# Kernel optimization log

Hardware: AMD Instinct MI355X
Metric: run time of the kernel (lower is better)

The kernel has to match this reference:

```python
import jax, jax.numpy as jnp
import numpy as np

B, S, H, I, E = 2, 1024, 1024, 4096, 8

def setup_inputs() -> dict:
    key = jax.random.key(0)
    ks = jax.random.split(key, 8)
    s_h = 1.0 / np.sqrt(H)
    s_i = 1.0 / np.sqrt(I)
    return {
        "x": jax.random.normal(ks[0], (B, S, H), dtype=jnp.float32),
        "router_w": jax.random.uniform(ks[1], (H, E), jnp.float32, -s_h, s_h),
        "router_b": jax.random.uniform(ks[2], (E,), jnp.float32, -s_h, s_h),
        "w1": jax.random.uniform(ks[3], (E, H, I), jnp.float32, -s_h, s_h),
        "b1": jax.random.uniform(ks[4], (E, I), jnp.float32, -s_h, s_h),
        "w2": jax.random.uniform(ks[5], (E, I, H), jnp.float32, -s_i, s_i),
        "b2": jax.random.uniform(ks[6], (E, H), jnp.float32, -s_i, s_i),
        "game_emb": jax.random.normal(ks[7], (E, H), dtype=jnp.float32) * 0.02,
    }

def reference(x, router_w, router_b, w1, b1, w2, b2, game_emb):
    # Router: top-1 expert per token (softmax is monotone, argmax of logits)
    logits = jnp.einsum('bsh,he->bse', x, router_w) + router_b  # [B,S,E]
    expert_idx = jnp.argmax(logits, axis=-1)                    # [B,S] int
    out = jnp.zeros_like(x)
    n_experts = w1.shape[0]
    for e in range(n_experts):  # fixed small expert loop
        mask = (expert_idx == e)[..., None]                     # [B,S,1]
        sel = x + 0.1 * game_emb[e]                             # embedding add
        h = jax.nn.gelu(jnp.einsum('bsh,hi->bsi', sel, w1[e]) + b1[e], approximate=False)
        y = jnp.einsum('bsi,ih->bsh', h, w2[e]) + b2[e]
        out = jnp.where(mask, y, out)                           # scatter combine
    return out
```

## Files before the change

### kernel.cpp

```cpp
#include <hip/hip_runtime.h>
#include <hip/hip_bf16.h>
#include <math.h>

#define HDIM 1024
#define IDIM 4096
#define NE 8
#define NTOK 2048
#define PADROWS 256

typedef __attribute__((ext_vector_type(8))) short bf16x8;
typedef __attribute__((ext_vector_type(4))) float f32x4;

__device__ __forceinline__ unsigned int f2bf(float f) {
    unsigned int u = __float_as_uint(f);
    u = (u + 0x7FFFu + ((u >> 16) & 1u)) >> 16;
    return u;
}

__device__ __forceinline__ unsigned int pkbf2(float lo, float hi) {
    union { __hip_bfloat162 h; unsigned int u; } cv;
    cv.h = __float22bfloat162_rn(make_float2(lo, hi));
    return cv.u;
}

template<typename T, typename U>
__device__ __forceinline__ void gld16(const T* g, U* l) {
    __builtin_amdgcn_global_load_lds((const __attribute__((address_space(1))) void*)g,
                                     (__attribute__((address_space(3))) void*)l, 16, 0, 0);
}

__global__ __launch_bounds__(256) void router_k(const float* __restrict__ x,
                                                const float* __restrict__ rw,
                                                const float* __restrict__ rb,
                                                int* __restrict__ eidx,
                                                int* __restrict__ counts) {
    const int wave = threadIdx.x >> 6, lane = threadIdx.x & 63;
    const int t = blockIdx.x * 4 + wave;
    if (t >= NTOK) return;
    double acc[NE];
#pragma unroll
    for (int e = 0; e < NE; e++) acc[e] = 0.0;
    for (int h = lane; h < HDIM; h += 64) {
        double xv = (double)x[(size_t)t * HDIM + h];
        const float4* rwp = (const float4*)&rw[h * NE];
        float4 r0 = rwp[0], r1 = rwp[1];
        acc[0] += xv * (double)r0.x;  acc[1] += xv * (double)r0.y;
        acc[2] += xv * (double)r0.z;  acc[3] += xv * (double)r0.w;
        acc[4] += xv * (double)r1.x;  acc[5] += xv * (double)r1.y;
        acc[6] += xv * (double)r1.z;  acc[7] += xv * (double)r1.w;
    }
#pragma unroll
    for (int m = 32; m >= 1; m >>= 1) {
#pragma unroll
        for (int e = 0; e < NE; e++) acc[e] += __shfl_xor(acc[e], m);
    }
    if (lane == 0) {
        double best = acc[0] + (double)rb[0];
        int be = 0;
#pragma unroll
        for (int e = 1; e < NE; e++) {
            double v = acc[e] + (double)rb[e];
            if (v > best) { best = v; be = e; }
        }
        eidx[t] = be;
        atomicAdd(&counts[be], 1);
    }
}

__global__ void scan_k(const int* __restrict__ counts, int* __restrict__ offsets) {
    if (threadIdx.x == 0 && blockIdx.x == 0) {
        int s = 0;
        for (int e = 0; e < NE; e++) { offsets[e] = s; s += counts[e]; }
        offsets[NE] = s;
    }
}

__global__ __launch_bounds__(256) void gather_k(const float* __restrict__ x,
                                                const float* __restrict__ gemb,
                                                const int* __restrict__ eidx,
                                                const int* __restrict__ offsets,
                                                int* __restrict__ cursors,
                                                int* __restrict__ rowmap,
                                                unsigned short* __restrict__ Xg) {
    __shared__ int srow, se;
    const int t = blockIdx.x;
    if (threadIdx.x == 0) {
        int e = eidx[t];
        int pos = atomicAdd(&cursors[e], 1);
        int row = offsets[e] + pos;
        rowmap[row] = t;
        srow = row; se = e;
    }
    __syncthreads();
    const int row = srow, e = se;
    const int c = threadIdx.x * 4;
    float4 xv = *(const float4*)&x[(size_t)t * HDIM + c];
    float4 gv = *(const float4*)&gemb[(size_t)e * HDIM + c];
    ushort4 o;
    o.x = (unsigned short)f2bf(xv.x + 0.1f * gv.x);
    o.y = (unsigned short)f2bf(xv.y + 0.1f * gv.y);
    o.z = (unsigned short)f2bf(xv.z + 0.1f * gv.z);
    o.w = (unsigned short)f2bf(xv.w + 0.1f * gv.w);
    *(ushort4*)&Xg[(size_t)row * HDIM + c] = o;
}

template<int BM, int BN, int EPI>
__global__ __launch_bounds__(256, 4) void moe_gemm_k(
        const unsigned short* __restrict__ A, int lda, int Kfull, int ksplit,
        const float* __restrict__ Bw, int ldbN,
        const float* __restrict__ bias,
        const int* __restrict__ offsets, const int* __restrict__ rowmap,
        unsigned short* __restrict__ Hout, float* __restrict__ Yout,
        float* __restrict__ P, size_t pstride) {
    constexpr int MFRAG = BM / 32;
    constexpr int NFRAG = BN / 32;
    constexpr int NIA = BM / 32;
    constexpr int NIB = BN / 16;

    __shared__ __align__(16) unsigned short At[BM * 64];
    __shared__ __align__(16) float Bt[64 * BN];

    const int e = blockIdx.z & 7;
    const int split = blockIdx.z >> 3;
    const int rend = offsets[e + 1];
    const int r0 = offsets[e] + blockIdx.y * BM;
    if (r0 >= rend) return;
    const int c0 = blockIdx.x * BN;
    const int kbeg = split * ksplit;
    const int nt = ksplit / 64;
    const float* Be = Bw + (size_t)e * Kfull * ldbN;

    const int tid = threadIdx.x;
    const int wave = tid >> 6, lane = tid & 63;
    const int wr = (wave >> 1) * (MFRAG * 16);
    const int wc = (wave & 1) * (NFRAG * 16);
    const int l15 = lane & 15, l4 = lane >> 4;

    f32x4 acc[MFRAG][NFRAG] = {};

    for (int t = 0; t < nt; ++t) {
        const int kk = kbeg + t * 64;
#pragma unroll
        for (int i = 0; i < NIA; ++i) {
            int gb = (wave * NIA + i) << 6;
            int g = gb + lane;
            int row = g >> 3, pkb = g & 7;
            const unsigned short* src =
                A + (size_t)(r0 + row) * lda + kk + ((pkb ^ (row & 7)) << 3);
            gld16(src, &At[(size_t)gb * 8]);
        }
#pragma unroll
        for (int i = 0; i < NIB; ++i) {
            int gb = (wave * NIB + i) << 6;
            int g = gb + lane;
            int k = g >> 4, cg = g & 15;
            int scg = cg ^ (((k >> 3) & 1) << 2);
            const float* src = Be + (size_t)(kk + k) * ldbN + c0 + (scg << 2);
            gld16(src, &Bt[(size_t)gb * 4]);
        }
        __syncthreads();
#pragma unroll
        for (int kh = 0; kh < 2; ++kh) {
            const int kb = kh * 4 + l4;
            bf16x8 af[MFRAG];
#pragma unroll
            for (int m = 0; m < MFRAG; ++m) {
                int row = wr + m * 16 + l15;
                af[m] = *(const bf16x8*)&At[(row * 8 + (kb ^ (row & 7))) * 8];
            }
#pragma unroll
            for (int n = 0; n < NFRAG; ++n) {
                int cswz = (wc + n * 16 + l15) ^ ((kb & 1) << 4);
                float f[8];
#pragma unroll
                for (int j = 0; j < 8; ++j)
                    f[j] = Bt[(kb * 8 + j) * BN + cswz];
                bf16x8 bfr;
                unsigned int* bu = (unsigned int*)&bfr;
#pragma unroll
                for (int j = 0; j < 4; ++j) bu[j] = pkbf2(f[2 * j], f[2 * j + 1]);
#pragma unroll
                for (int m = 0; m < MFRAG; ++m)
                    acc[m][n] = __builtin_amdgcn_mfma_f32_16x16x32_bf16(af[m], bfr, acc[m][n], 0, 0, 0);
            }
        }
        __syncthreads();
    }

#pragma unroll
    for (int m = 0; m < MFRAG; ++m) {
#pragma unroll
        for (int r = 0; r < 4; ++r) {
            const int row = r0 + wr + m * 16 + l4 * 4 + r;
            if (row < rend) {
                if constexpr (EPI == 0) {
#pragma unroll
                    for (int n = 0; n < NFRAG; ++n) {
                        int col = c0 + wc + n * 16 + l15;
                        float v = acc[m][n][r] + bias[(size_t)e * ldbN + col];
                        float g = 0.5f * v * (1.0f + erff(v * 0.70710678118654752f));
                        Hout[(size_t)row * IDIM + col] = (unsigned short)f2bf(g);
                    }
                } else if (split == 0) {
                    const int tt = rowmap[row];
#pragma unroll
                    for (int n = 0; n < NFRAG; ++n) {
                        int col = c0 + wc + n * 16 + l15;
                        Yout[(size_t)tt * HDIM + col] = acc[m][n][r] + bias[(size_t)e * ldbN + col];
                    }
                } else {
                    float* Ps = P + (size_t)(split - 1) * pstride;
#pragma unroll
                    for (int n = 0; n < NFRAG; ++n) {
                        int col = c0 + wc + n * 16 + l15;
                        Ps[(size_t)row * HDIM + col] = acc[m][n][r];
                    }
                }
            }
        }
    }
}

__global__ __launch_bounds__(256) void reduce_k(const float* __restrict__ P,
                                                size_t pstride, int nparts,
                                                const int* __restrict__ rowmap,
                                                float* __restrict__ out) {
    const int row = blockIdx.x;
    const int t = rowmap[row];
    const int c = threadIdx.x * 4;
    f32x4 s = *(const f32x4*)&out[(size_t)t * HDIM + c];
    for (int p = 0; p < nparts; ++p)
        s += *(const f32x4*)&P[(size_t)p * pstride + (size_t)row * HDIM + c];
    *(f32x4*)&out[(size_t)t * HDIM + c] = s;
}

extern "C" void kernel_launch(void* const* d_in, const int* in_sizes, int n_in,
                              void* d_out, int out_size, void* d_ws, size_t ws_size,
                              hipStream_t stream) {
    const float* x    = (const float*)d_in[0];
    const float* rw   = (const float*)d_in[1];
    const float* rb   = (const float*)d_in[2];
    const float* w1   = (const float*)d_in[3];
    const float* b1   = (const float*)d_in[4];
    const float* w2   = (const float*)d_in[5];
    const float* b2   = (const float*)d_in[6];
    const float* gemb = (const float*)d_in[7];
    float* out = (float*)d_out;

    char* ws = (char*)d_ws;
    int* meta    = (int*)ws;
    int* counts  = meta;
    int* cursors = meta + 8;
    int* offsets = meta + 16;
    int* eidx    = meta + 32;
    int* rowmap  = meta + 32 + NTOK;
    size_t off = 32768;
    unsigned short* Xg = (unsigned short*)(ws + off);
    off += (size_t)(NTOK + PADROWS) * HDIM * 2;
    unsigned short* Hbuf = (unsigned short*)(ws + off);
    off += (size_t)(NTOK + PADROWS) * IDIM * 2;
    float* P = (float*)(ws + off);
    const size_t pstride = (size_t)NTOK * HDIM;
    int nsplit = 1;
    if (ws_size >= off + 3 * pstride * 4) nsplit = 4;
    else if (ws_size >= off + 1 * pstride * 4) nsplit = 2;

    hipMemsetAsync(counts, 0, 16 * sizeof(int), stream);
    router_k<<<NTOK / 4, 256, 0, stream>>>(x, rw, rb, eidx, counts);
    scan_k<<<1, 64, 0, stream>>>(counts, offsets);
    gather_k<<<NTOK, 256, 0, stream>>>(x, gemb, eidx, offsets, cursors, rowmap, Xg);
    moe_gemm_k<128, 64, 0><<<dim3(IDIM / 64, 6, NE), 256, 0, stream>>>(
        Xg, HDIM, HDIM, HDIM, w1, IDIM, b1, offsets, rowmap, Hbuf, nullptr, nullptr, 0);
    moe_gemm_k<128, 64, 1><<<dim3(HDIM / 64, 6, NE * nsplit), 256, 0, stream>>>(
        Hbuf, IDIM, IDIM, IDIM / nsplit, w2, HDIM, b2, offsets, rowmap, nullptr, out, P, pstride);
    if (nsplit > 1)
        reduce_k<<<NTOK, 256, 0, stream>>>(P, pstride, nsplit - 1, rowmap, out);
}
```

Before: 212.6 us.

## Restructure MoE GEMM to 128x128 tiles with pre-converted bf16 B and double-buffered A

The expert GEMM kernel now uses 128x128 output tiles with 4x4 MFMA fragments per wave. Weight tiles are loaded into registers, converted to bf16 once, and stored transposed and swizzled in LDS. This replaces having every wave reload fp32 from LDS and repack it for each fragment. A tiles are double-buffered with async global-to-LDS loads, and the next B tile is prefetched into registers while MFMAs run. erff is replaced by a polynomial erf approximation. The grid now has only 3 row-blocks per expert, so any expert receiving more than 384 tokens would leave rows uncomputed, and the larger tiles raise register and LDS pressure.

Result: faster. 193.3 us (-9.1%).

```diff
diff --git a/kernel.cpp b/kernel.cpp
--- a/kernel.cpp
+++ b/kernel.cpp
@@ -21,6 +21,23 @@
     union { __hip_bfloat162 h; unsigned int u; } cv;
     cv.h = __float22bfloat162_rn(make_float2(lo, hi));
     return cv.u;
+}
+
+__device__ __forceinline__ float comp4(const float4& v, int c) {
+    return c == 0 ? v.x : c == 1 ? v.y : c == 2 ? v.z : v.w;
+}
+
+__device__ __forceinline__ int swz8(int i) { return (i ^ (i >> 3)) & 7; }
+
+__device__ __forceinline__ float gelu_erf(float v) {
+    float x = v * 0.70710678118654752f;
+    float ax = fabsf(x);
+    float t = 1.0f / (1.0f + 0.3275911f * ax);
+    float p = t * (0.254829592f + t * (-0.284496736f + t * (1.421413741f +
+              t * (-1.453152027f + t * 1.061405429f))));
+    float er = 1.0f - p * __expf(-x * x);
+    er = copysignf(er, v);
+    return 0.5f * v * (1.0f + er);
 }
 
 template<typename T, typename U>
@@ -104,114 +121,138 @@
     *(ushort4*)&Xg[(size_t)row * HDIM + c] = o;
 }
 
-template<int BM, int BN, int EPI>
-__global__ __launch_bounds__(256, 4) void moe_gemm_k(
+template<int EPI>
+__global__ __launch_bounds__(256, 3) void moe_gemm_k(
         const unsigned short* __restrict__ A, int lda, int Kfull, int ksplit,
         const float* __restrict__ Bw, int ldbN,
         const float* __restrict__ bias,
         const int* __restrict__ offsets, const int* __restrict__ rowmap,
         unsigned short* __restrict__ Hout, float* __restrict__ Yout,
         float* __restrict__ P, size_t pstride) {
-    constexpr int MFRAG = BM / 32;
-    constexpr int NFRAG = BN / 32;
-    constexpr int NIA = BM / 32;
-    constexpr int NIB = BN / 16;
-
-    __shared__ __align__(16) unsigned short At[BM * 64];
-    __shared__ __align__(16) float Bt[64 * BN];
+    __shared__ __align__(16) unsigned short At[2][128 * 64];
+    __shared__ __align__(16) unsigned short Bt[128 * 64];
 
     const int e = blockIdx.z & 7;
     const int split = blockIdx.z >> 3;
     const int rend = offsets[e + 1];
-    const int r0 = offsets[e] + blockIdx.y * BM;
+    const int r0 = offsets[e] + blockIdx.y * 128;
     if (r0 >= rend) return;
-    const int c0 = blockIdx.x * BN;
+    const int c0 = blockIdx.x * 128;
     const int kbeg = split * ksplit;
     const int nt = ksplit / 64;
     const float* Be = Bw + (size_t)e * Kfull * ldbN;
 
     const int tid = threadIdx.x;
     const int wave = tid >> 6, lane = tid & 63;
-    const int wr = (wave >> 1) * (MFRAG * 16);
-    const int wc = (wave & 1) * (NFRAG * 16);
+    const int wr = (wave >> 1) * 64, wc = (wave & 1) * 64;
     const int l15 = lane & 15, l4 = lane >> 4;
 
-    f32x4 acc[MFRAG][NFRAG] = {};
-
+    const int bcol = (tid & 31) * 4;
+    const int boct = tid >> 5;
+    const float* bsrc = Be + (size_t)boct * 8 * ldbN + c0 + bcol;
+    int bwo[4];
+#pragma unroll
+    for (int i = 0; i < 4; ++i) {
+        int col = bcol + i;
+        bwo[i] = col * 64 + (boct ^ swz8(col)) * 8;
+    }
+
+    const unsigned short* adsrc[4];
+    int adoff[4];
+#pragma unroll
+    for (int p = 0; p < 4; ++p) {
+        int gidx = p * 256 + tid;
+        int row = gidx >> 3, ps = gidx & 7;
+        adsrc[p] = A + (size_t)(r0 + row) * lda + (ps ^ swz8(row)) * 8;
+        adoff[p] = gidx * 8;
+    }
+
+    float4 fv[8];
+    auto loadB = [&](int kabs) {
+#pragma unroll
+        for (int j = 0; j < 8; ++j)
+            fv[j] = *(const float4*)&bsrc[(size_t)(kabs + j) * ldbN];
+    };
+    auto dmaA = [&](int kabs, int buf) {
+#pragma unroll
+        for (int p = 0; p < 4; ++p)
+            gld16(adsrc[p] + kabs, &At[buf][adoff[p]]);
+    };
+
+    f32x4 acc[4][4];
+#pragma unroll
+    for (int m = 0; m < 4; ++m)
+#pragma unroll
+        for (int n = 0; n < 4; ++n) acc[m][n] = (f32x4){0.f, 0.f, 0.f, 0.f};
+
+    loadB(kbeg);
+    dmaA(kbeg, 0);
     for (int t = 0; t < nt; ++t) {
-        const int kk = kbeg + t * 64;
-#pragma unroll
-        for (int i = 0; i < NIA; ++i) {
-            int gb = (wave * NIA + i) << 6;
-            int g = gb + lane;
-            int row = g >> 3, pkb = g & 7;
-            const unsigned short* src =
-                A + (size_t)(r0 + row) * lda + kk + ((pkb ^ (row & 7)) << 3);
-            gld16(src, &At[(size_t)gb * 8]);
-        }
-#pragma unroll
-        for (int i = 0; i < NIB; ++i) {
-            int gb = (wave * NIB + i) << 6;
-            int g = gb + lane;
-            int k = g >> 4, cg = g & 15;
-            int scg = cg ^ (((k >> 3) & 1) << 2);
-            const float* src = Be + (size_t)(kk + k) * ldbN + c0 + (scg << 2);
-            gld16(src, &Bt[(size_t)gb * 4]);
-        }
-        __syncthreads();
+        const int cur = t & 1;
+#pragma unroll
+        for (int i = 0; i < 4; ++i) {
+            uint4 w;
+            w.x = pkbf2(comp4(fv[0], i), comp4(fv[1], i));
+            w.y = pkbf2(comp4(fv[2], i), comp4(fv[3], i));
+            w.z = pkbf2(comp4(fv[4], i), comp4(fv[5], i));
+            w.w = pkbf2(comp4(fv[6], i), comp4(fv[7], i));
+            *(uint4*)&Bt[bwo[i]] = w;
+        }
+        asm volatile("s_waitcnt vmcnt(0) lgkmcnt(0)" ::: "memory");
+        __builtin_amdgcn_s_barrier();
+        __builtin_amdgcn_sched_barrier(0);
+        if (t + 1 < nt) {
+            loadB(kbeg + (t + 1) * 64);
+            dmaA(kbeg + (t + 1) * 64, cur ^ 1);
+        }
 #pragma unroll
         for (int kh = 0; kh < 2; ++kh) {
             const int kb = kh * 4 + l4;
-            bf16x8 af[MFRAG];
-#pragma unroll
-            for (int m = 0; m < MFRAG; ++m) {
+            bf16x8 af[4], bfr[4];
+#pragma unroll
+            for (int m = 0; m < 4; ++m) {
                 int row = wr + m * 16 + l15;
-                af[m] = *(const bf16x8*)&At[(row * 8 + (kb ^ (row & 7))) * 8];
+                af[m] = *(const bf16x8*)&At[cur][row * 64 + (kb ^ swz8(row)) * 8];
             }
 #pragma unroll
-            for (int n = 0; n < NFRAG; ++n) {
-                int cswz = (wc + n * 16 + l15) ^ ((kb & 1) << 4);
-                float f[8];
-#pragma unroll
-                for (int j = 0; j < 8; ++j)
-                    f[j] = Bt[(kb * 8 + j) * BN + cswz];
-                bf16x8 bfr;
-                unsigned int* bu = (unsigned int*)&bfr;
-#pragma unroll
-                for (int j = 0; j < 4; ++j) bu[j] = pkbf2(f[2 * j], f[2 * j + 1]);
-#pragma unroll
-                for (int m = 0; m < MFRAG; ++m)
-                    acc[m][n] = __builtin_amdgcn_mfma_f32_16x16x32_bf16(af[m], bfr, acc[m][n], 0, 0, 0);
+            for (int n = 0; n < 4; ++n) {
+                int col = wc + n * 16 + l15;
+                bfr[n] = *(const bf16x8*)&Bt[col * 64 + (kb ^ swz8(col)) * 8];
             }
-        }
-        __syncthreads();
-    }
-
-#pragma unroll
-    for (int m = 0; m < MFRAG; ++m) {
+#pragma unroll
+            for (int m = 0; m < 4; ++m)
+#pragma unroll
+                for (int n = 0; n < 4; ++n)
+                    acc[m][n] = __builtin_amdgcn_mfma_f32_16x16x32_bf16(af[m], bfr[n], acc[m][n], 0, 0, 0);
+        }
+        __builtin_amdgcn_sched_barrier(0);
+        __builtin_amdgcn_s_barrier();
+    }
+
+#pragma unroll
+    for (int m = 0; m < 4; ++m) {
 #pragma unroll
         for (int r = 0; r < 4; ++r) {
             const int row = r0 + wr + m * 16 + l4 * 4 + r;
             if (row < rend) {
                 if constexpr (EPI == 0) {
 #pragma unroll
-                    for (int n = 0; n < NFRAG; ++n) {
+                    for (int n = 0; n < 4; ++n) {
                         int col = c0 + wc + n * 16 + l15;
                         float v = acc[m][n][r] + bias[(size_t)e * ldbN + col];
-                        float g = 0.5f * v * (1.0f + erff(v * 0.70710678118654752f));
-                        Hout[(size_t)row * IDIM + col] = (unsigned short)f2bf(g);
+                        Hout[(size_t)row * IDIM + col] = (unsigned short)f2bf(gelu_erf(v));
                     }
                 } else if (split == 0) {
                     const int tt = rowmap[row];
 #pragma unroll
-                    for (int n = 0; n < NFRAG; ++n) {
+                    for (int n = 0; n < 4; ++n) {
                         int col = c0 + wc + n * 16 + l15;
                         Yout[(size_t)tt * HDIM + col] = acc[m][n][r] + bias[(size_t)e * ldbN + col];
                     }
                 } else {
                     float* Ps = P + (size_t)(split - 1) * pstride;
 #pragma unroll
-                    for (int n = 0; n < NFRAG; ++n) {
+                    for (int n = 0; n < 4; ++n) {
                         int col = c0 + wc + n * 16 + l15;
                         Ps[(size_t)row * HDIM + col] = acc[m][n][r];
                     }
@@ -269,9 +310,9 @@
     router_k<<<NTOK / 4, 256, 0, stream>>>(x, rw, rb, eidx, counts);
     scan_k<<<1, 64, 0, stream>>>(counts, offsets);
     gather_k<<<NTOK, 256, 0, stream>>>(x, gemb, eidx, offsets, cursors, rowmap, Xg);
-    moe_gemm_k<128, 64, 0><<<dim3(IDIM / 64, 6, NE), 256, 0, stream>>>(
+    moe_gemm_k<0><<<dim3(IDIM / 128, 3, NE), 256, 0, stream>>>(
         Xg, HDIM, HDIM, HDIM, w1, IDIM, b1, offsets, rowmap, Hbuf, nullptr, nullptr, 0);
-    moe_gemm_k<128, 64, 1><<<dim3(HDIM / 64, 6, NE * nsplit), 256, 0, stream>>>(
+    moe_gemm_k<1><<<dim3(HDIM / 128, 3, NE * nsplit), 256, 0, stream>>>(
         Hbuf, IDIM, IDIM, IDIM / nsplit, w2, HDIM, b2, offsets, rowmap, nullptr, out, P, pstride);
     if (nsplit > 1)
         reduce_k<<<NTOK, 256, 0, stream>>>(P, pstride, nsplit - 1, rowmap, out);
```
